# Performance work log

Measured on AMD Instinct MI355X. Metric: run time of the kernel, lower is better.

The kernel has to match this reference:

```python
import jax, jax.numpy as jnp
import numpy as np

N_SEND = 49152   # 12 * 64^2 HEALPix nodes
N_REC = 65536    # 256x256 receiver grid
N_EDGES = 262144 # N_REC * 4 nearest senders
D_MODEL = 256
EDGE_IN, EDGE_OUT = 4, 64
LIN_IN, LIN_OUT = 320, 256
B = 2


def setup_inputs() -> dict:
    key = jax.random.key(0)
    ks = jax.random.split(key, 8)
    x = jax.random.normal(ks[0], (B, N_SEND, D_MODEL), dtype=jnp.float32)
    senders = jax.random.randint(ks[1], (N_EDGES,), 0, N_SEND, dtype=jnp.int32)
    receivers = jax.random.randint(ks[2], (N_EDGES,), 0, N_REC, dtype=jnp.int32)
    edge_index = jnp.stack([senders, receivers], axis=0)
    edge_attr = jax.random.normal(ks[3], (N_EDGES, EDGE_IN), dtype=jnp.float32)
    s = lambda fan_in: 1.0 / np.sqrt(fan_in)
    return {
        "x": x,
        "edge_index": edge_index,
        "edge_attr": edge_attr,
        "ee_w1": jax.random.normal(ks[4], (EDGE_IN, EDGE_OUT), dtype=jnp.float32) * s(EDGE_IN),
        "ee_b1": jnp.zeros((EDGE_OUT,), dtype=jnp.float32),
        "ee_w2": jax.random.normal(ks[5], (EDGE_OUT, EDGE_OUT), dtype=jnp.float32) * s(EDGE_OUT),
        "ee_b2": jnp.zeros((EDGE_OUT,), dtype=jnp.float32),
        "ff_w1": jax.random.normal(ks[6], (LIN_IN, LIN_OUT), dtype=jnp.float32) * s(LIN_IN),
        "ff_b1": jnp.zeros((LIN_OUT,), dtype=jnp.float32),
        "ff_w2": jax.random.normal(ks[7], (LIN_OUT, LIN_OUT), dtype=jnp.float32) * s(LIN_OUT),
        "ff_b2": jnp.zeros((LIN_OUT,), dtype=jnp.float32),
    }


def reference(x, edge_index, edge_attr,
              ee_w1, ee_b1, ee_w2, ee_b2,
              ff_w1, ff_b1, ff_w2, ff_b2):
    senders, receivers = edge_index[0], edge_index[1]
    # edge embedder MLP: [E, edge_in] -> [E, edge_out]
    h = jax.nn.relu(edge_attr @ ee_w1 + ee_b1)
    edge_feat = h @ ee_w2 + ee_b2                       # [E, edge_out]
    # gather sender node features: [B, E, d_model]
    v_s = x[:, senders, :]
    # concat with broadcast edge features: [B, E, d_model + edge_out]
    ef = jnp.broadcast_to(edge_feat[None], (x.shape[0],) + edge_feat.shape)
    v_s_prime = jnp.concatenate([v_s, ef], axis=-1)
    # scatter-sum onto receiver nodes: [B, n_rec, lin_in]
    v_m_sum = jnp.zeros((x.shape[0], N_REC, v_s_prime.shape[-1]), dtype=x.dtype)
    v_m_sum = v_m_sum.at[:, receivers, :].add(v_s_prime)
    # g2m feedforward: [B, n_rec, lin_out]
    h2 = jax.nn.relu(v_m_sum @ ff_w1 + ff_b1)
    return h2 @ ff_w2 + ff_b2
```

## Files before the change

kernel.cpp:

```cpp
#include <hip/hip_runtime.h>
#include <hip/hip_bf16.h>

#define N_SEND 49152
#define N_REC  65536
#define N_EDGES 262144
#define D_MODEL 256
#define EDGE_IN 4
#define EDGE_OUT 64
#define LIN_IN 320
#define LIN_OUT 256
#define BATCH 2

#define GBM 64

typedef __attribute__((ext_vector_type(4))) float f32x4;
typedef __attribute__((ext_vector_type(8))) short bf16x8;

static __device__ __forceinline__ unsigned short f2bf(float f) {
    union { float f; unsigned u; } v; v.f = f;
    unsigned r = v.u + 0x7FFF + ((v.u >> 16) & 1);
    return (unsigned short)(r >> 16);
}
static __device__ __forceinline__ float bf2f(unsigned short h) {
    union { unsigned u; float f; } v; v.u = ((unsigned)h) << 16; return v.f;
}

static __device__ __forceinline__ void async_copy16(void* lds_ptr, const void* g_ptr) {
    __builtin_amdgcn_global_load_lds(
        (const __attribute__((address_space(1))) void*)g_ptr,
        (__attribute__((address_space(3))) void*)lds_ptr, 16, 0, 0);
}

__global__ __launch_bounds__(256) void prep_fused(
    const float* __restrict__ x, unsigned short* __restrict__ xb, int nconv,
    const int* __restrict__ receivers, const float* __restrict__ edge_attr,
    const float* __restrict__ ee_w1, const float* __restrict__ ee_b1,
    const float* __restrict__ ee_w2, const float* __restrict__ ee_b2,
    unsigned short* __restrict__ efs, int* __restrict__ counts,
    const float* __restrict__ w1, const float* __restrict__ w2,
    unsigned short* __restrict__ w1t, unsigned short* __restrict__ w2t)
{
    __shared__ __align__(16) unsigned short h_lds[256 * EDGE_OUT];

    const int bid = blockIdx.x;
    const int tid = threadIdx.x;

    if (bid < nconv) {
        const size_t i = ((size_t)bid * 256 + tid) * 8;
        const float4 v0 = *(const float4*)&x[i];
        const float4 v1 = *(const float4*)&x[i + 4];
        bf16x8 o;
        o[0] = (short)f2bf(v0.x); o[1] = (short)f2bf(v0.y);
        o[2] = (short)f2bf(v0.z); o[3] = (short)f2bf(v0.w);
        o[4] = (short)f2bf(v1.x); o[5] = (short)f2bf(v1.y);
        o[6] = (short)f2bf(v1.z); o[7] = (short)f2bf(v1.w);
        *(bf16x8*)&xb[i] = o;
        return;
    }
    const int b2 = bid - nconv;

    if (b2 < N_EDGES / 256) {
        const int e0 = b2 * 256;
        atomicAdd(&counts[receivers[e0 + tid]], 1);

        {
            const float4 ea = *(const float4*)&edge_attr[(size_t)(e0 + tid) * EDGE_IN];
#pragma unroll
            for (int kb = 0; kb < 8; ++kb) {
                bf16x8 hv;
#pragma unroll
                for (int j = 0; j < 8; ++j) {
                    const int k = kb * 8 + j;
                    float a = ee_b1[k];
                    a += ea.x * ee_w1[0 * EDGE_OUT + k];
                    a += ea.y * ee_w1[1 * EDGE_OUT + k];
                    a += ea.z * ee_w1[2 * EDGE_OUT + k];
                    a += ea.w * ee_w1[3 * EDGE_OUT + k];
                    hv[j] = (short)f2bf(fmaxf(a, 0.0f));
                }
                *(bf16x8*)&h_lds[tid * EDGE_OUT + ((kb ^ (tid & 7)) * 8)] = hv;
            }
        }

        const int lane = tid & 63, wave = tid >> 6;
        const int n16 = lane & 15, hi = lane >> 4;

        bf16x8 bfr[2][4];
#pragma unroll
        for (int ch = 0; ch < 2; ++ch)
#pragma unroll
            for (int c = 0; c < 4; ++c) {
                bf16x8 b;
#pragma unroll
                for (int j = 0; j < 8; ++j) {
                    const int k = ch * 32 + hi * 8 + j;
                    b[j] = (short)f2bf(ee_w2[k * EDGE_OUT + 16 * c + n16]);
                }
                bfr[ch][c] = b;
            }

        f32x4 acc[4][4];
#pragma unroll
        for (int c = 0; c < 4; ++c) {
            const float bv = ee_b2[16 * c + n16];
#pragma unroll
            for (int t = 0; t < 4; ++t) {
                acc[t][c][0] = bv; acc[t][c][1] = bv; acc[t][c][2] = bv; acc[t][c][3] = bv;
            }
        }

#pragma unroll
        for (int ch = 0; ch < 2; ++ch) {
            bf16x8 af[4];
#pragma unroll
            for (int t = 0; t < 4; ++t) {
                const int row = 64 * wave + 16 * t + n16;
                const int slot = (4 * ch + hi) ^ (row & 7);
                af[t] = *(const bf16x8*)&h_lds[row * EDGE_OUT + slot * 8];
            }
#pragma unroll
            for (int c = 0; c < 4; ++c)
#pragma unroll
                for (int t = 0; t < 4; ++t)
                    acc[t][c] = __builtin_amdgcn_mfma_f32_16x16x32_bf16(af[t], bfr[ch][c], acc[t][c], 0, 0, 0);
        }

#pragma unroll
        for (int t = 0; t < 4; ++t)
#pragma unroll
            for (int c = 0; c < 4; ++c)
#pragma unroll
                for (int r = 0; r < 4; ++r)
                    efs[(size_t)(e0 + 64 * wave + 16 * t + 4 * hi + r) * EDGE_OUT + 16 * c + n16] =
                        f2bf(acc[t][c][r]);
        return;
    }

    {
        const int t3 = (b2 - N_EDGES / 256) * 256 + tid;
        if (t3 < 256 * LIN_IN) {
            const int n = t3 / LIN_IN, k = t3 - n * LIN_IN;
            w1t[t3] = f2bf(w1[k * LIN_OUT + n]);
        } else {
            const int t2 = t3 - 256 * LIN_IN;
            if (t2 < 256 * 256) {
                const int n = t2 >> 8, k = t2 & 255;
                w2t[t2] = f2bf(w2[k * LIN_OUT + n]);
            }
        }
    }
}

__global__ __launch_bounds__(1024) void scan_kernel(
    const int* __restrict__ counts, int* __restrict__ row_ptr,
    int* __restrict__ cursor)
{
    __shared__ int sums[1024];
    const int t = threadIdx.x;
    const int4* c4 = (const int4*)(counts + t * 64);

    int s = 0;
#pragma unroll
    for (int i = 0; i < 16; ++i) { const int4 c = c4[i]; s += c.x + c.y + c.z + c.w; }
    sums[t] = s;
    __syncthreads();

    for (int off = 1; off < 1024; off <<= 1) {
        const int v = (t >= off) ? sums[t - off] : 0;
        __syncthreads();
        sums[t] += v;
        __syncthreads();
    }

    int run = sums[t] - s;
#pragma unroll
    for (int i = 0; i < 16; ++i) {
        const int4 c = c4[i];
        int4 w;
        w.x = run; w.y = run + c.x; w.z = w.y + c.y; w.w = w.z + c.z;
        run = w.w + c.w;
        ((int4*)(row_ptr + t * 64))[i] = w;
        ((int4*)(cursor + t * 64))[i] = w;
    }
    if (t == 1023) row_ptr[N_REC] = run;
}

__global__ __launch_bounds__(256) void fill_kernel(
    const int* __restrict__ senders, const int* __restrict__ receivers,
    int* __restrict__ cursor, int* __restrict__ edge_order,
    int* __restrict__ ssort)
{
    const int e = blockIdx.x * 256 + threadIdx.x;
    const int r = receivers[e];
    const int pos = atomicAdd(&cursor[r], 1);
    edge_order[pos] = e;
    ssort[pos] = senders[e];
}

__global__ __launch_bounds__(256) void gather_kernel(
    const unsigned short* __restrict__ xb,
    const unsigned short* __restrict__ efs,
    const int* __restrict__ row_ptr,
    const int* __restrict__ edge_order,
    const int* __restrict__ ssort,
    unsigned short* __restrict__ vmb)
{
    const int lane = threadIdx.x & 63;
    const int wave = threadIdx.x >> 6;
    const int r = blockIdx.x * 4 + wave;
    const int beg = row_ptr[r], end = row_ptr[r + 1];
    const int half = lane >> 5, l2 = lane & 31;
    const size_t xbase = (size_t)half * N_SEND * D_MODEL;

    float ax[8] = {0, 0, 0, 0, 0, 0, 0, 0};
    float ae[8] = {0, 0, 0, 0, 0, 0, 0, 0};

    for (int chunk = beg; chunk < end; chunk += 64) {
        const int n = min(64, end - chunk);
        int myidx = 0, myeidx = 0;
        if (chunk + lane < end) {
            myidx = ssort[chunk + lane];
            myeidx = edge_order[chunk + lane];
        }
        for (int i = 0; i < n; i += 4) {
            bf16x8 vx[4], ve[4];
#pragma unroll
            for (int u = 0; u < 4; ++u) {
                const int s = __shfl(myidx, i + u);
                const int e = __shfl(myeidx, i + u);
                const bool p = (i + u < n);
                const bf16x8 z = {0, 0, 0, 0, 0, 0, 0, 0};
                vx[u] = z; ve[u] = z;
                if (p) vx[u] = *(const bf16x8*)&xb[xbase + (size_t)s * D_MODEL + l2 * 8];
                if (p && lane < 8) ve[u] = *(const bf16x8*)&efs[(size_t)e * EDGE_OUT + lane * 8];
            }
#pragma unroll
            for (int u = 0; u < 4; ++u)
#pragma unroll
                for (int j = 0; j < 8; ++j)
                    ax[j] += bf2f((unsigned short)vx[u][j]);
            if (lane < 8) {
#pragma unroll
                for (int u = 0; u < 4; ++u)
#pragma unroll
                    for (int j = 0; j < 8; ++j)
                        ae[j] += bf2f((unsigned short)ve[u][j]);
            }
        }
    }

    bf16x8 o;
#pragma unroll
    for (int j = 0; j < 8; ++j) o[j] = (short)f2bf(ax[j]);
    *(bf16x8*)&vmb[((size_t)(half * N_REC + r)) * LIN_IN + l2 * 8] = o;
    if (lane < 8) {
        bf16x8 oe;
#pragma unroll
        for (int j = 0; j < 8; ++j) oe[j] = (short)f2bf(ae[j]);
        *(bf16x8*)&vmb[((size_t)r) * LIN_IN + D_MODEL + lane * 8] = oe;
        *(bf16x8*)&vmb[((size_t)(N_REC + r)) * LIN_IN + D_MODEL + lane * 8] = oe;
    }
}

__global__ __launch_bounds__(256, 2) void node_mlp_fused(
    const unsigned short* __restrict__ vmb,
    const unsigned short* __restrict__ w1t,
    const float* __restrict__ b1,
    const unsigned short* __restrict__ w2t,
    const float* __restrict__ b2,
    float* __restrict__ out)
{
    __shared__ __align__(16) char lds[73728];

    const int tid  = threadIdx.x;
    const int lane = tid & 63, wc = tid >> 6;
    const int n16  = lane & 15, hi = lane >> 4;
    const size_t row0 = (size_t)blockIdx.x * GBM;
    char* const hbase = lds + 40960;

    const int f_l = (n16 & 3) ^ ((n16 >> 2) & 3);
    const int hsl = (hi ^ f_l) << 4;

    auto stageA = [&](int kk, int buf) {
        const int row = tid >> 2;
        const int sl = (tid & 3) ^ ((row & 3) ^ ((row >> 2) & 3));
        const unsigned short* g = vmb + (row0 + row) * LIN_IN + kk + sl * 8;
        char* l = lds + (buf << 12) + ((tid >> 6) << 10);
        async_copy16(l, g);
    };
    auto stageB = [&](const unsigned short* BT, int ldk, int kk, int buf) {
#pragma unroll
        for (int p = 0; p < 4; ++p) {
            const int i = p * 256 + tid, row = i >> 2;
            const int sl = (i & 3) ^ ((row & 3) ^ ((row >> 2) & 3));
            const unsigned short* g = BT + (size_t)row * ldk + kk + sl * 8;
            char* l = lds + 8192 + (buf << 14) + (p << 12) + ((tid >> 6) << 10);
            async_copy16(l, g);
        }
    };

    stageA(0, 0); stageB(w1t, LIN_IN, 0, 0);

    f32x4 acc[4][4];
#pragma unroll
    for (int c = 0; c < 4; ++c) {
        const float bv = b1[64 * wc + 16 * c + n16];
#pragma unroll
        for (int t = 0; t < 4; ++t) {
            acc[t][c][0] = bv; acc[t][c][1] = bv; acc[t][c][2] = bv; acc[t][c][3] = bv;
        }
    }

    int cur = 0;
    for (int step = 0; step < LIN_IN / 32; ++step) {
        __syncthreads();
        if (step + 1 < LIN_IN / 32) {
            stageA((step + 1) * 32, cur ^ 1);
            stageB(w1t, LIN_IN, (step + 1) * 32, cur ^ 1);
        }
        bf16x8 af[4], bf[4];
        const char* Ab = lds + (cur << 12);
        const char* Bb = lds + 8192 + (cur << 14);
#pragma unroll
        for (int t = 0; t < 4; ++t)
            af[t] = *(const bf16x8*)(Ab + (16 * t + n16) * 64 + hsl);
#pragma unroll
        for (int c = 0; c < 4; ++c)
            bf[c] = *(const bf16x8*)(Bb + (64 * wc + 16 * c + n16) * 64 + hsl);
#pragma unroll
        for (int c = 0; c < 4; ++c)
#pragma unroll
            for (int t = 0; t < 4; ++t)
                acc[t][c] = __builtin_amdgcn_mfma_f32_16x16x32_bf16(af[t], bf[c], acc[t][c], 0, 0, 0);
        cur ^= 1;
    }

    stageB(w2t, LIN_OUT, 0, 0);

#pragma unroll
    for (int t = 0; t < 4; ++t)
#pragma unroll
        for (int c = 0; c < 4; ++c) {
            const int col = 64 * wc + 16 * c + n16;
            const int kc = col >> 5;
            const int b  = (col & 31) * 2;
            const int gslot = b >> 4;
#pragma unroll
            for (int r = 0; r < 4; ++r) {
                const int lrow = 16 * t + 4 * hi + r;
                const int f = (lrow & 3) ^ ((lrow >> 2) & 3);
                *(unsigned short*)(hbase + (kc << 12) + lrow * 64 + (((gslot ^ f) << 4) | (b & 15))) =
                    f2bf(fmaxf(acc[t][c][r], 0.0f));
            }
        }
    __syncthreads();

    f32x4 acc2[4][4];
#pragma unroll
    for (int c = 0; c < 4; ++c) {
        const float bv = b2[64 * wc + 16 * c + n16];
#pragma unroll
        for (int t = 0; t < 4; ++t) {
            acc2[t][c][0] = bv; acc2[t][c][1] = bv; acc2[t][c][2] = bv; acc2[t][c][3] = bv;
        }
    }

    cur = 0;
    for (int step = 0; step < LIN_OUT / 32; ++step) {
        if (step + 1 < LIN_OUT / 32) stageB(w2t, LIN_OUT, (step + 1) * 32, cur ^ 1);

        bf16x8 af[4], bf[4];
        const char* Hb = hbase + (step << 12);
        const char* Bb = lds + 8192 + (cur << 14);
#pragma unroll
        for (int t = 0; t < 4; ++t)
            af[t] = *(const bf16x8*)(Hb + (16 * t + n16) * 64 + hsl);
#pragma unroll
        for (int c = 0; c < 4; ++c)
            bf[c] = *(const bf16x8*)(Bb + (64 * wc + 16 * c + n16) * 64 + hsl);
#pragma unroll
        for (int c = 0; c < 4; ++c)
#pragma unroll
            for (int t = 0; t < 4; ++t)
                acc2[t][c] = __builtin_amdgcn_mfma_f32_16x16x32_bf16(af[t], bf[c], acc2[t][c], 0, 0, 0);

        __syncthreads();
        cur ^= 1;
    }

#pragma unroll
    for (int t = 0; t < 4; ++t)
#pragma unroll
        for (int c = 0; c < 4; ++c)
#pragma unroll
            for (int r = 0; r < 4; ++r)
                out[(row0 + 16 * t + 4 * hi + r) * LIN_OUT + 64 * wc + 16 * c + n16] =
                    acc2[t][c][r];
}

extern "C" void kernel_launch(void* const* d_in, const int* in_sizes, int n_in,
                              void* d_out, int out_size, void* d_ws, size_t ws_size,
                              hipStream_t stream) {
    const float* x         = (const float*)d_in[0];
    const int*   edge_idx  = (const int*)d_in[1];
    const float* edge_attr = (const float*)d_in[2];
    const float* ee_w1     = (const float*)d_in[3];
    const float* ee_b1     = (const float*)d_in[4];
    const float* ee_w2     = (const float*)d_in[5];
    const float* ee_b2     = (const float*)d_in[6];
    const float* ff_w1     = (const float*)d_in[7];
    const float* ff_b1     = (const float*)d_in[8];
    const float* ff_w2     = (const float*)d_in[9];
    const float* ff_b2     = (const float*)d_in[10];
    float* out = (float*)d_out;

    const int* senders   = edge_idx;
    const int* receivers = edge_idx + N_EDGES;

    char* ws = (char*)d_ws;
    size_t off = 0;
    auto alloc = [&](size_t bytes) { char* p = ws + off; off += (bytes + 511) & ~511ull; return p; };

    unsigned short* vmb = (unsigned short*)alloc((size_t)BATCH * N_REC * LIN_IN * 2);
    unsigned short* efs = (unsigned short*)alloc((size_t)N_EDGES * EDGE_OUT * 2);
    unsigned short* xb  = (unsigned short*)alloc((size_t)BATCH * N_SEND * D_MODEL * 2);
    unsigned short* w1t = (unsigned short*)alloc((size_t)256 * LIN_IN * 2);
    unsigned short* w2t = (unsigned short*)alloc((size_t)256 * LIN_OUT * 2);
    int* row_ptr        = (int*)alloc((size_t)(N_REC + 1) * 4);
    int* counts         = (int*)alloc((size_t)N_REC * 4);
    int* cursor         = (int*)alloc((size_t)N_REC * 4);
    int* edge_order     = (int*)alloc((size_t)N_EDGES * 4);
    int* ssort          = (int*)alloc((size_t)N_EDGES * 4);

    hipMemsetAsync(counts, 0, (size_t)N_REC * 4, stream);

    const int nconv = (int)((size_t)BATCH * N_SEND * D_MODEL / 8 / 256);
    const int prep_grid = nconv + N_EDGES / 256 + (256 * LIN_IN + 256 * LIN_OUT + 255) / 256;
    prep_fused<<<prep_grid, 256, 0, stream>>>(
        x, xb, nconv, receivers, edge_attr, ee_w1, ee_b1, ee_w2, ee_b2,
        efs, counts, ff_w1, ff_w2, w1t, w2t);

    scan_kernel<<<1, 1024, 0, stream>>>(counts, row_ptr, cursor);

    fill_kernel<<<N_EDGES / 256, 256, 0, stream>>>(
        senders, receivers, cursor, edge_order, ssort);

    gather_kernel<<<N_REC / 4, 256, 0, stream>>>(
        xb, efs, row_ptr, edge_order, ssort, vmb);

    node_mlp_fused<<<(BATCH * N_REC) / GBM, 256, 0, stream>>>(
        vmb, w1t, ff_b1, w2t, ff_b2, out);
}
```

Before: 242.6 us.

## Preload full A tile and give each wave private weight buffers to drop barriers

The fused node MLP kernel now loads the whole 64x320 activation tile into LDS at the start. Each wave streams only its own 64-column slice of the weights into a private double buffer. Because no wave reads data staged by another wave inside the K loops, the per-step __syncthreads are replaced by per-wave vmcnt waits, leaving only barriers around the hidden-activation handoff. The hidden activations reuse the A region. This lowers block-wide synchronisation stalls, but the hand-written waitcnt counts and LDS aliasing are fragile and could introduce races if they are wrong.

```diff
diff --git a/kernel.cpp b/kernel.cpp
--- a/kernel.cpp
+++ b/kernel.cpp
@@ -276,30 +276,34 @@
     const int lane = tid & 63, wc = tid >> 6;
     const int n16  = lane & 15, hi = lane >> 4;
     const size_t row0 = (size_t)blockIdx.x * GBM;
-    char* const hbase = lds + 40960;
+    char* const wB = lds + 40960 + wc * 8192;
 
     const int f_l = (n16 & 3) ^ ((n16 >> 2) & 3);
     const int hsl = (hi ^ f_l) << 4;
 
-    auto stageA = [&](int kk, int buf) {
+    auto stageA = [&](int kc) {
         const int row = tid >> 2;
         const int sl = (tid & 3) ^ ((row & 3) ^ ((row >> 2) & 3));
-        const unsigned short* g = vmb + (row0 + row) * LIN_IN + kk + sl * 8;
-        char* l = lds + (buf << 12) + ((tid >> 6) << 10);
+        const unsigned short* g = vmb + (row0 + row) * LIN_IN + kc * 32 + sl * 8;
+        char* l = lds + (kc << 12) + ((tid >> 6) << 10);
         async_copy16(l, g);
     };
-    auto stageB = [&](const unsigned short* BT, int ldk, int kk, int buf) {
+    auto issueB = [&](const unsigned short* BT, int ldk, int kk, int buf) {
 #pragma unroll
         for (int p = 0; p < 4; ++p) {
-            const int i = p * 256 + tid, row = i >> 2;
+            const int i = p * 64 + lane;
+            const int row = i >> 2;
             const int sl = (i & 3) ^ ((row & 3) ^ ((row >> 2) & 3));
-            const unsigned short* g = BT + (size_t)row * ldk + kk + sl * 8;
-            char* l = lds + 8192 + (buf << 14) + (p << 12) + ((tid >> 6) << 10);
+            const unsigned short* g = BT + (size_t)(64 * wc + row) * ldk + kk + sl * 8;
+            char* l = wB + (buf << 12) + (p << 10);
             async_copy16(l, g);
         }
     };
 
-    stageA(0, 0); stageB(w1t, LIN_IN, 0, 0);
+#pragma unroll
+    for (int kc = 0; kc < LIN_IN / 32; ++kc) stageA(kc);
+    issueB(w1t, LIN_IN, 0, 0);
+    __syncthreads();
 
     f32x4 acc[4][4];
 #pragma unroll
@@ -311,31 +315,37 @@
         }
     }
 
-    int cur = 0;
+    int buf = 0;
     for (int step = 0; step < LIN_IN / 32; ++step) {
-        __syncthreads();
         if (step + 1 < LIN_IN / 32) {
-            stageA((step + 1) * 32, cur ^ 1);
-            stageB(w1t, LIN_IN, (step + 1) * 32, cur ^ 1);
-        }
+            issueB(w1t, LIN_IN, (step + 1) * 32, buf ^ 1);
+            __builtin_amdgcn_sched_barrier(0);
+            asm volatile("s_waitcnt vmcnt(4)" ::: "memory");
+        } else {
+            asm volatile("s_waitcnt vmcnt(0)" ::: "memory");
+        }
+        __builtin_amdgcn_sched_barrier(0);
+
         bf16x8 af[4], bf[4];
-        const char* Ab = lds + (cur << 12);
-        const char* Bb = lds + 8192 + (cur << 14);
+        const char* Ab = lds + (step << 12);
+        const char* Bb = wB + (buf << 12);
 #pragma unroll
         for (int t = 0; t < 4; ++t)
             af[t] = *(const bf16x8*)(Ab + (16 * t + n16) * 64 + hsl);
 #pragma unroll
         for (int c = 0; c < 4; ++c)
-            bf[c] = *(const bf16x8*)(Bb + (64 * wc + 16 * c + n16) * 64 + hsl);
+            bf[c] = *(const bf16x8*)(Bb + (16 * c + n16) * 64 + hsl);
 #pragma unroll
         for (int c = 0; c < 4; ++c)
 #pragma unroll
             for (int t = 0; t < 4; ++t)
                 acc[t][c] = __builtin_amdgcn_mfma_f32_16x16x32_bf16(af[t], bf[c], acc[t][c], 0, 0, 0);
-        cur ^= 1;
-    }
-
-    stageB(w2t, LIN_OUT, 0, 0);
+        buf ^= 1;
+    }
+
+    __syncthreads();
+
+    issueB(w2t, LIN_OUT, 0, 0);
 
 #pragma unroll
     for (int t = 0; t < 4; ++t)
@@ -349,11 +359,13 @@
             for (int r = 0; r < 4; ++r) {
                 const int lrow = 16 * t + 4 * hi + r;
                 const int f = (lrow & 3) ^ ((lrow >> 2) & 3);
-                *(unsigned short*)(hbase + (kc << 12) + lrow * 64 + (((gslot ^ f) << 4) | (b & 15))) =
+                *(unsigned short*)(lds + (kc << 12) + lrow * 64 + (((gslot ^ f) << 4) | (b & 15))) =
                     f2bf(fmaxf(acc[t][c][r], 0.0f));
             }
         }
-    __syncthreads();
+    asm volatile("s_waitcnt lgkmcnt(0)" ::: "memory");
+    __builtin_amdgcn_s_barrier();
+    __builtin_amdgcn_sched_barrier(0);
 
     f32x4 acc2[4][4];
 #pragma unroll
@@ -365,27 +377,32 @@
         }
     }
 
-    cur = 0;
+    buf = 0;
     for (int step = 0; step < LIN_OUT / 32; ++step) {
-        if (step + 1 < LIN_OUT / 32) stageB(w2t, LIN_OUT, (step + 1) * 32, cur ^ 1);
+        if (step + 1 < LIN_OUT / 32) {
+            issueB(w2t, LIN_OUT, (step + 1) * 32, buf ^ 1);
+            __builtin_amdgcn_sched_barrier(0);
+            asm volatile("s_waitcnt vmcnt(4)" ::: "memory");
+        } else {
+            asm volatile("s_waitcnt vmcnt(0)" ::: "memory");
+        }
+        __builtin_amdgcn_sched_barrier(0);
 
         bf16x8 af[4], bf[4];
-        const char* Hb = hbase + (step << 12);
-        const char* Bb = lds + 8192 + (cur << 14);
+        const char* Hb = lds + (step << 12);
+        const char* Bb = wB + (buf << 12);
 #pragma unroll
         for (int t = 0; t < 4; ++t)
             af[t] = *(const bf16x8*)(Hb + (16 * t + n16) * 64 + hsl);
 #pragma unroll
         for (int c = 0; c < 4; ++c)
-            bf[c] = *(const bf16x8*)(Bb + (64 * wc + 16 * c + n16) * 64 + hsl);
+            bf[c] = *(const bf16x8*)(Bb + (16 * c + n16) * 64 + hsl);
 #pragma unroll
         for (int c = 0; c < 4; ++c)
 #pragma unroll
             for (int t = 0; t < 4; ++t)
                 acc2[t][c] = __builtin_amdgcn_mfma_f32_16x16x32_bf16(af[t], bf[c], acc2[t][c], 0, 0, 0);
-
-        __syncthreads();
-        cur ^= 1;
+        buf ^= 1;
     }
 
 #pragma unroll
```

Measured after the change: 238.0 us. About the same (-1.9%).

## Load weights directly into registers and stage full A tile in LDS

Applied to the files above, without the earlier changes.

The fused node MLP kernel no longer stages weight tiles through LDS. Each wave now reads its B fragments straight from global memory (L2-resident weights) into registers, using a two-buffer register prefetch. The whole 64x320 A tile is loaded into LDS up front with a single barrier, and the hidden activations reuse the same LDS region. This cuts LDS from 72KB to 40KB and raises launch bounds to 4 blocks per CU, trading LDS traffic and per-step barriers for uncoalesced global loads and more register pressure.

```diff
diff --git a/kernel.cpp b/kernel.cpp
--- a/kernel.cpp
+++ b/kernel.cpp
@@ -262,7 +262,7 @@
     }
 }
 
-__global__ __launch_bounds__(256, 2) void node_mlp_fused(
+__global__ __launch_bounds__(256, 4) void node_mlp_fused(
     const unsigned short* __restrict__ vmb,
     const unsigned short* __restrict__ w1t,
     const float* __restrict__ b1,
@@ -270,36 +270,31 @@
     const float* __restrict__ b2,
     float* __restrict__ out)
 {
-    __shared__ __align__(16) char lds[73728];
+    __shared__ __align__(16) char lds[40960];
 
     const int tid  = threadIdx.x;
     const int lane = tid & 63, wc = tid >> 6;
     const int n16  = lane & 15, hi = lane >> 4;
     const size_t row0 = (size_t)blockIdx.x * GBM;
-    char* const hbase = lds + 40960;
 
     const int f_l = (n16 & 3) ^ ((n16 >> 2) & 3);
     const int hsl = (hi ^ f_l) << 4;
 
-    auto stageA = [&](int kk, int buf) {
+    auto stageA = [&](int kc) {
         const int row = tid >> 2;
         const int sl = (tid & 3) ^ ((row & 3) ^ ((row >> 2) & 3));
-        const unsigned short* g = vmb + (row0 + row) * LIN_IN + kk + sl * 8;
-        char* l = lds + (buf << 12) + ((tid >> 6) << 10);
+        const unsigned short* g = vmb + (row0 + row) * LIN_IN + kc * 32 + sl * 8;
+        char* l = lds + (kc << 12) + ((tid >> 6) << 10);
         async_copy16(l, g);
     };
-    auto stageB = [&](const unsigned short* BT, int ldk, int kk, int buf) {
-#pragma unroll
-        for (int p = 0; p < 4; ++p) {
-            const int i = p * 256 + tid, row = i >> 2;
-            const int sl = (i & 3) ^ ((row & 3) ^ ((row >> 2) & 3));
-            const unsigned short* g = BT + (size_t)row * ldk + kk + sl * 8;
-            char* l = lds + 8192 + (buf << 14) + (p << 12) + ((tid >> 6) << 10);
-            async_copy16(l, g);
-        }
+    auto loadB = [&](const unsigned short* BT, int ldk, int kk, bf16x8 (&bf)[4]) {
+#pragma unroll
+        for (int c = 0; c < 4; ++c)
+            bf[c] = *(const bf16x8*)&BT[(size_t)(64 * wc + 16 * c + n16) * ldk + kk + hi * 8];
     };
 
-    stageA(0, 0); stageB(w1t, LIN_IN, 0, 0);
+#pragma unroll
+    for (int kc = 0; kc < LIN_IN / 32; ++kc) stageA(kc);
 
     f32x4 acc[4][4];
 #pragma unroll
@@ -311,31 +306,33 @@
         }
     }
 
-    int cur = 0;
-    for (int step = 0; step < LIN_IN / 32; ++step) {
-        __syncthreads();
-        if (step + 1 < LIN_IN / 32) {
-            stageA((step + 1) * 32, cur ^ 1);
-            stageB(w1t, LIN_IN, (step + 1) * 32, cur ^ 1);
-        }
-        bf16x8 af[4], bf[4];
-        const char* Ab = lds + (cur << 12);
-        const char* Bb = lds + 8192 + (cur << 14);
+    bf16x8 bP[4], bQ[4];
+    loadB(w1t, LIN_IN, 0, bP);
+    __syncthreads();
+
+    auto mstep = [&](const char* Ab, bf16x8 (&bf)[4], f32x4 (&ac)[4][4]) {
+        bf16x8 af[4];
 #pragma unroll
         for (int t = 0; t < 4; ++t)
             af[t] = *(const bf16x8*)(Ab + (16 * t + n16) * 64 + hsl);
 #pragma unroll
         for (int c = 0; c < 4; ++c)
-            bf[c] = *(const bf16x8*)(Bb + (64 * wc + 16 * c + n16) * 64 + hsl);
-#pragma unroll
-        for (int c = 0; c < 4; ++c)
 #pragma unroll
             for (int t = 0; t < 4; ++t)
-                acc[t][c] = __builtin_amdgcn_mfma_f32_16x16x32_bf16(af[t], bf[c], acc[t][c], 0, 0, 0);
-        cur ^= 1;
-    }
-
-    stageB(w2t, LIN_OUT, 0, 0);
+                ac[t][c] = __builtin_amdgcn_mfma_f32_16x16x32_bf16(af[t], bf[c], ac[t][c], 0, 0, 0);
+    };
+
+#pragma unroll
+    for (int s = 0; s < LIN_IN / 32; s += 2) {
+        loadB(w1t, LIN_IN, (s + 1) * 32, bQ);
+        mstep(lds + (s << 12), bP, acc);
+        if (s + 2 < LIN_IN / 32) loadB(w1t, LIN_IN, (s + 2) * 32, bP);
+        mstep(lds + ((s + 1) << 12), bQ, acc);
+    }
+
+    __syncthreads();
+
+    loadB(w2t, LIN_OUT, 0, bP);
 
 #pragma unroll
     for (int t = 0; t < 4; ++t)
@@ -349,7 +346,7 @@
             for (int r = 0; r < 4; ++r) {
                 const int lrow = 16 * t + 4 * hi + r;
                 const int f = (lrow & 3) ^ ((lrow >> 2) & 3);
-                *(unsigned short*)(hbase + (kc << 12) + lrow * 64 + (((gslot ^ f) << 4) | (b & 15))) =
+                *(unsigned short*)(lds + (kc << 12) + lrow * 64 + (((gslot ^ f) << 4) | (b & 15))) =
                     f2bf(fmaxf(acc[t][c][r], 0.0f));
             }
         }
@@ -365,27 +362,12 @@
         }
     }
 
-    cur = 0;
-    for (int step = 0; step < LIN_OUT / 32; ++step) {
-        if (step + 1 < LIN_OUT / 32) stageB(w2t, LIN_OUT, (step + 1) * 32, cur ^ 1);
-
-        bf16x8 af[4], bf[4];
-        const char* Hb = hbase + (step << 12);
-        const char* Bb = lds + 8192 + (cur << 14);
-#pragma unroll
-        for (int t = 0; t < 4; ++t)
-            af[t] = *(const bf16x8*)(Hb + (16 * t + n16) * 64 + hsl);
-#pragma unroll
-        for (int c = 0; c < 4; ++c)
-            bf[c] = *(const bf16x8*)(Bb + (64 * wc + 16 * c + n16) * 64 + hsl);
-#pragma unroll
-        for (int c = 0; c < 4; ++c)
-#pragma unroll
-            for (int t = 0; t < 4; ++t)
-                acc2[t][c] = __builtin_amdgcn_mfma_f32_16x16x32_bf16(af[t], bf[c], acc2[t][c], 0, 0, 0);
-
-        __syncthreads();
-        cur ^= 1;
+#pragma unroll
+    for (int s = 0; s < LIN_OUT / 32; s += 2) {
+        loadB(w2t, LIN_OUT, (s + 1) * 32, bQ);
+        mstep(lds + (s << 12), bP, acc2);
+        if (s + 2 < LIN_OUT / 32) loadB(w2t, LIN_OUT, (s + 2) * 32, bP);
+        mstep(lds + ((s + 1) << 12), bQ, acc2);
     }
 
 #pragma unroll
```

Result: slower. 279.5 us (+15.2%).
